# Optimization experiments

Measured on AMD Instinct MI355X. Metric: run time of the kernel, lower is better.

## Reference

```python
import jax, jax.numpy as jnp
import numpy as np

N = 100000       # nodes
E = 3200000      # edges (before self loops)
EMB = 16         # embedding dim (EMB_SIZE)
H = 32           # hidden_size
NUM_EMB = 141
EDGE_DIM = 1     # NUM_EDGE_FEATURES
NEG_SLOPE = 0.2  # PyG GATConv default negative_slope


def setup_inputs() -> dict:
    key = jax.random.key(0)
    ks = jax.random.split(key, 18)
    f32 = jnp.float32
    return {
        "x_idx": jax.random.randint(ks[0], (N, 1), 0, NUM_EMB),
        "edge_index": jax.random.randint(ks[1], (2, E), 0, N),
        "edge_attr": jax.random.normal(ks[2], (E, EDGE_DIM), f32),
        # learned params
        "emb": jax.random.normal(ks[3], (NUM_EMB, EMB), f32) * 0.1,
        # conv1 (GATConv 16->32, heads=1, edge_dim=1)
        "W1": jax.random.normal(ks[4], (EMB, H), f32) * (1.0 / np.sqrt(EMB)),
        "as1": jax.random.normal(ks[5], (H,), f32) * 0.1,
        "ad1": jax.random.normal(ks[6], (H,), f32) * 0.1,
        "We1": jax.random.normal(ks[7], (EDGE_DIM, H), f32),
        "ae1": jax.random.normal(ks[8], (H,), f32) * 0.1,
        "b1": jnp.zeros((H,), f32),
        # conv2 (GATConv 32->32)
        "W2": jax.random.normal(ks[9], (H, H), f32) * (1.0 / np.sqrt(H)),
        "as2": jax.random.normal(ks[10], (H,), f32) * 0.1,
        "ad2": jax.random.normal(ks[11], (H,), f32) * 0.1,
        "We2": jax.random.normal(ks[12], (EDGE_DIM, H), f32),
        "ae2": jax.random.normal(ks[13], (H,), f32) * 0.1,
        "b2": jnp.zeros((H,), f32),
        # linear head 32->1
        "Wl": jax.random.normal(ks[14], (H, 1), f32) * (1.0 / np.sqrt(H)),
        "bl": jnp.zeros((1,), f32),
    }


def _add_self_loops(src, dst, ea):
    # PyG add_self_loops with fill_value='mean': loop edge_attr is the
    # segment-mean of incoming edge_attr per destination node.
    sums = jax.ops.segment_sum(ea, dst, num_segments=N)            # [N, EDGE_DIM]
    cnts = jax.ops.segment_sum(jnp.ones((ea.shape[0],), ea.dtype), dst, num_segments=N)
    loop_attr = sums / jnp.maximum(cnts, 1.0)[:, None]
    loop = jnp.arange(N, dtype=src.dtype)
    return (jnp.concatenate([src, loop]),
            jnp.concatenate([dst, loop]),
            jnp.concatenate([ea, loop_attr], axis=0))


def _gat_conv(x, src, dst, ea, W, a_s, a_d, We, a_e, b):
    h = x @ W                                   # [N, H]
    e = ea @ We                                 # [E2, H]
    alpha = jax.nn.leaky_relu((h @ a_s)[src] + (h @ a_d)[dst] + e @ a_e, NEG_SLOPE)
    # segment softmax over incoming edges of each dst node
    amax = jax.ops.segment_max(alpha, dst, num_segments=N)
    ex = jnp.exp(alpha - amax[dst])
    denom = jax.ops.segment_sum(ex, dst, num_segments=N)
    coef = ex / (denom[dst] + 1e-16)            # [E2]
    out = jax.ops.segment_sum(h[src] * coef[:, None], dst, num_segments=N)
    return out + b


def reference(x_idx, edge_index, edge_attr, emb, W1, as1, ad1, We1, ae1, b1,
              W2, as2, ad2, We2, ae2, b2, Wl, bl):
    src, dst, ea = _add_self_loops(edge_index[0], edge_index[1], edge_attr)
    x = emb[x_idx[:, 0]]                        # [N, EMB]
    x = _gat_conv(x, src, dst, ea, W1, as1, ad1, We1, ae1, b1)
    x = jax.nn.relu(x)                          # dropout is identity in eval mode
    x = _gat_conv(x, src, dst, ea, W2, as2, ad2, We2, ae2, b2)
    return x @ Wl + bl                          # [N, 1]
```

## Files before the change

### kernel.cpp

```cpp
#include <hip/hip_runtime.h>

#define NN 100000
#define NE 3200000
#define H 32
#define EMBD 16
#define NEMB 141
#define NEG_SLOPE 0.2f
#define CSH 7
#define CN 128
#define NCO 782
#define CAP 4608
#define LCAP 4608
#define KCH 12800
#define GA 250

__device__ __forceinline__ float bf2f(unsigned short u) {
    return __int_as_float((int)u << 16);
}

__global__ void k_tab(const float* __restrict__ emb, const float* __restrict__ W1,
                      const float* __restrict__ as1, const float* __restrict__ ad1,
                      const float* We1, const float* ae1,
                      const float* We2, const float* ae2,
                      const float* W2, const float* as2, const float* ad2,
                      const float* Wl, const float* b2, const float* bl,
                      float* tabH, float* tabS, float* tabD, float* scal,
                      float* was2, float* wad2, float* wl2, float* c0,
                      int* bcnt) {
    int gid = blockIdx.x * 64 + threadIdx.x;
    if (gid < NCO) bcnt[gid] = 0;
    int r = blockIdx.x, j = threadIdx.x;
    if (j >= 32) {
        if (r == 0 && j == 32) {
            float c1 = 0.f, c2 = 0.f;
            for (int k = 0; k < H; k++) {
                c1 += We1[k] * ae1[k];
                c2 += We2[k] * ae2[k];
            }
            scal[0] = c1; scal[1] = c2;
        }
        if (r == 1) {
            int k = j - 32;
            float s = 0.f, d = 0.f, l = 0.f;
            for (int q = 0; q < H; q++) {
                float w = W2[k * H + q];
                s += w * as2[q];
                d += w * ad2[q];
                l += w * Wl[q];
            }
            was2[k] = s; wad2[k] = d; wl2[k] = l;
        }
        if (r == 2 && j == 32) {
            float c = bl[0];
            for (int q = 0; q < H; q++) c += b2[q] * Wl[q];
            c0[0] = c;
        }
        return;
    }
    float acc = 0.f;
    #pragma unroll
    for (int k = 0; k < EMBD; k++) acc += emb[r * EMBD + k] * W1[k * H + j];
    tabH[r * H + j] = acc;
    float s = acc * as1[j];
    float d = acc * ad1[j];
    #pragma unroll
    for (int off = 16; off > 0; off >>= 1) {
        s += __shfl_down(s, off, 32);
        d += __shfl_down(d, off, 32);
    }
    if (j == 0) { tabS[r] = s; tabD[r] = d; }
}

__global__ __launch_bounds__(1024) void k_pscat(
                        const int* __restrict__ src, const int* __restrict__ dst,
                        const float* __restrict__ ea, const int* __restrict__ x_idx,
                        int* bcnt, long long* epk) {
    __shared__ long long st[KCH];
    __shared__ unsigned short cbuk[KCH];
    __shared__ int hist[NCO];
    __shared__ int scanb[1024];
    __shared__ int bas[NCO];
    __shared__ int allow[NCO];
    int t = threadIdx.x;
    int e0 = blockIdx.x * KCH;
    const int4*   d4 = (const int4*)(dst + e0);
    const int4*   s4 = (const int4*)(src + e0);
    const float4* a4 = (const float4*)(ea + e0);
    if (t < NCO) hist[t] = 0;
    __syncthreads();

    long long pkr[4][4];
    int       pcr[4][4];
    #pragma unroll
    for (int g = 0; g < 4; g++) {
        bool v = (g < 3) || (t < 128);
        if (v) {
            int gi = g * 1024 + t;
            int4 d = d4[gi];
            int4 s = s4[gi];
            float4 a = a4[gi];
            int x0 = x_idx[s.x], x1 = x_idx[s.y], x2 = x_idx[s.z], x3 = x_idx[s.w];
            int c0 = d.x >> CSH, c1 = d.y >> CSH, c2 = d.z >> CSH, c3 = d.w >> CSH;
            pkr[g][0] = ((long long)(unsigned)__float_as_int(a.x) << 32)
                      | (unsigned)(s.x | ((d.x & (CN - 1)) << 17) | (x0 << 24));
            pkr[g][1] = ((long long)(unsigned)__float_as_int(a.y) << 32)
                      | (unsigned)(s.y | ((d.y & (CN - 1)) << 17) | (x1 << 24));
            pkr[g][2] = ((long long)(unsigned)__float_as_int(a.z) << 32)
                      | (unsigned)(s.z | ((d.z & (CN - 1)) << 17) | (x2 << 24));
            pkr[g][3] = ((long long)(unsigned)__float_as_int(a.w) << 32)
                      | (unsigned)(s.w | ((d.w & (CN - 1)) << 17) | (x3 << 24));
            pcr[g][0] = (c0 << 14) | atomicAdd(&hist[c0], 1);
            pcr[g][1] = (c1 << 14) | atomicAdd(&hist[c1], 1);
            pcr[g][2] = (c2 << 14) | atomicAdd(&hist[c2], 1);
            pcr[g][3] = (c3 << 14) | atomicAdd(&hist[c3], 1);
        }
    }
    __syncthreads();

    int hv = (t < NCO) ? hist[t] : 0;
    scanb[t] = hv;
    __syncthreads();
    for (int s = 1; s < 1024; s <<= 1) {
        int x = (t >= s) ? scanb[t - s] : 0;
        __syncthreads();
        scanb[t] += x;
        __syncthreads();
    }
    scanb[t] -= hv;
    if (t < NCO) {
        if (hv) {
            int b = atomicAdd(&bcnt[t], hv);
            bas[t]   = t * CAP + b;
            allow[t] = CAP - b;
        } else {
            bas[t] = t * CAP; allow[t] = 0;
        }
    }
    __syncthreads();

    #pragma unroll
    for (int g = 0; g < 4; g++) {
        bool v = (g < 3) || (t < 128);
        if (v) {
            #pragma unroll
            for (int e = 0; e < 4; e++) {
                int c = pcr[g][e] >> 14;
                int r = pcr[g][e] & 0x3fff;
                int pos = scanb[c] + r;
                st[pos] = pkr[g][e];
                cbuk[pos] = (unsigned short)c;
            }
        }
    }
    __syncthreads();

    for (int i = t; i < KCH; i += 1024) {
        int c = cbuk[i];
        int l = i - scanb[c];
        if (l < allow[c]) epk[bas[c] + l] = st[i];
    }
}

__global__ void k_psort(const int* __restrict__ bcnt, long long* epk, int2* nfo) {
    __shared__ long long st[LCAP];
    __shared__ unsigned short rnk[LCAP];
    __shared__ int hist[CN], lofs[CN];
    int c = blockIdx.x, t = threadIdx.x;
    int base = c * CAP;
    int cnt = bcnt[c];
    if (cnt > CAP) cnt = CAP;
    if (t < CN) hist[t] = 0;
    __syncthreads();
    for (int k = t; k < cnt; k += 512) {
        long long pk = epk[base + k];
        st[k] = pk;
        rnk[k] = (unsigned short)atomicAdd(&hist[((int)pk >> 17) & (CN - 1)], 1);
    }
    __syncthreads();
    if (t < CN) lofs[t] = hist[t];
    __syncthreads();
    for (int s = 1; s < CN; s <<= 1) {
        int x = (t >= s && t < CN) ? lofs[t - s] : 0;
        __syncthreads();
        if (t < CN) lofs[t] += x;
        __syncthreads();
    }
    if (t < CN) {
        int ex = lofs[t] - hist[t];
        lofs[t] = ex;
        int node = c * CN + t;
        if (node < NN) nfo[node] = make_int2(base + ex, hist[t]);
    }
    __syncthreads();
    for (int k = t; k < cnt; k += 512) {
        long long pk = st[k];
        int ln = ((int)pk >> 17) & (CN - 1);
        epk[base + lofs[ln] + rnk[k]] = pk;
    }
}

__global__ void k_agg1(const int2* __restrict__ nfo, const long long* __restrict__ epk,
                       const float* __restrict__ tabS, const float* __restrict__ tabD,
                       const float* __restrict__ scal,
                       const float* __restrict__ tabH,
                       const int* __restrict__ xi,
                       const float* __restrict__ bias,
                       const float* __restrict__ was2, const float* __restrict__ wad2,
                       const float* __restrict__ wl2,
                       float2* __restrict__ g2, float* __restrict__ hd2) {
    int lane = threadIdx.x & 31;
    int node = (blockIdx.x * blockDim.x + threadIdx.x) >> 5;
    if (node >= NN) return;
    int2 fo = nfo[node];
    int beg = fo.x;
    int dg  = fo.y;
    int end = beg + dg;
    float sc = scal[0];
    int xin = xi[node];
    float hdi = tabD[xin];

    float suma = 0.f, denp = 0.f, acc = 0.f;
    int base = beg;
    for (; end - base > 16; base += 32) {
        int kk = base + lane;
        int pw = 0;
        if (kk < end) {
            long long pk = epk[kk];
            int lo = (int)pk;
            float a = __int_as_float((int)(pk >> 32));
            suma += a;
            float hsv = tabS[(lo >> 24) & 0xff];
            float al = hsv + hdi + sc * a;
            al = (al > 0.f) ? al : NEG_SLOPE * al;
            int eb = __float_as_int(__expf(al));
            pw = ((eb + 0x80) & 0xffffff00) | ((lo >> 24) & 0xff);
            denp += __int_as_float(pw & 0xffffff00);
        }
        #pragma unroll
        for (int t = 0; t < 32; t++) {
            int p = __shfl(pw, t, 32);
            float ext = __int_as_float(p & 0xffffff00);
            float hv  = tabH[(p & 0xff) * H + lane];
            acc += ext * hv;
        }
    }
    if (base < end) {
        int kk = base + lane;
        int pw = 0;
        if (kk < end) {
            long long pk = epk[kk];
            int lo = (int)pk;
            float a = __int_as_float((int)(pk >> 32));
            suma += a;
            float hsv = tabS[(lo >> 24) & 0xff];
            float al = hsv + hdi + sc * a;
            al = (al > 0.f) ? al : NEG_SLOPE * al;
            int eb = __float_as_int(__expf(al));
            pw = ((eb + 0x80) & 0xffffff00) | ((lo >> 24) & 0xff);
            denp += __int_as_float(pw & 0xffffff00);
        }
        #pragma unroll
        for (int t = 0; t < 16; t++) {
            int p = __shfl(pw, t, 32);
            float ext = __int_as_float(p & 0xffffff00);
            float hv  = tabH[(p & 0xff) * H + lane];
            acc += ext * hv;
        }
    }
    #pragma unroll
    for (int o = 16; o > 0; o >>= 1) {
        suma += __shfl_xor(suma, o, 32);
        denp += __shfl_xor(denp, o, 32);
    }
    float la = suma / (float)((dg > 0) ? dg : 1);
    float alself = tabS[xin] + hdi + sc * la;
    alself = (alself > 0.f) ? alself : NEG_SLOPE * alself;
    float exs = __expf(alself);
    acc += exs * tabH[xin * H + lane];
    float den = denp + exs + 1e-16f;
    float u = acc / den;

    float x = fmaxf(u + bias[lane], 0.f);
    float sp = x * was2[lane];
    float dp = x * wad2[lane];
    float yp = x * wl2[lane];
    #pragma unroll
    for (int o = 16; o > 0; o >>= 1) {
        sp += __shfl_xor(sp, o, 32);
        dp += __shfl_xor(dp, o, 32);
        yp += __shfl_xor(yp, o, 32);
    }
    if (lane == 0) { g2[node] = make_float2(sp, yp); hd2[node] = dp; }
}

__global__ void k_agg2(const int2* __restrict__ nfo, const long long* __restrict__ epk,
                       const float2* __restrict__ g2, const float* __restrict__ hd2,
                       const float* __restrict__ scal, const float* __restrict__ c0p,
                       float* __restrict__ outF) {
    int lane = threadIdx.x & 31;
    int node = (blockIdx.x * blockDim.x + threadIdx.x) >> 5;
    if (node >= NN) return;
    int2 fo = nfo[node];
    int beg = fo.x;
    int dg  = fo.y;
    int end = beg + dg;
    float sc = scal[1];
    float hdi = hd2[node];
    float2 gn = g2[node];

    float num = 0.f, den = 0.f, suma = 0.f;
    for (int base = beg; base < end; base += 32) {
        int kk = base + lane;
        if (kk < end) {
            long long pk = epk[kk];
            float a = __int_as_float((int)(pk >> 32));
            int s = (int)pk & 0x1ffff;
            float2 g = g2[s];
            suma += a;
            float al = g.x + hdi + sc * a;
            al = (al > 0.f) ? al : NEG_SLOPE * al;
            float ex = __expf(al);
            num += ex * g.y;
            den += ex;
        }
    }
    #pragma unroll
    for (int o = 16; o > 0; o >>= 1) {
        num  += __shfl_xor(num, o, 32);
        den  += __shfl_xor(den, o, 32);
        suma += __shfl_xor(suma, o, 32);
    }
    float la = suma / (float)((dg > 0) ? dg : 1);
    float als = gn.x + hdi + sc * la;
    als = (als > 0.f) ? als : NEG_SLOPE * als;
    float exs = __expf(als);
    num += exs * gn.y;
    den += exs + 1e-16f;
    if (lane == 0) outF[node] = num / den + c0p[0];
}

extern "C" void kernel_launch(void* const* d_in, const int* in_sizes, int n_in,
                              void* d_out, int out_size, void* d_ws, size_t ws_size,
                              hipStream_t stream) {
    const int*   x_idx = (const int*)d_in[0];
    const int*   src   = (const int*)d_in[1];
    const int*   dst   = src + NE;
    const float* ea    = (const float*)d_in[2];
    const float* emb = (const float*)d_in[3];
    const float* W1  = (const float*)d_in[4];
    const float* as1 = (const float*)d_in[5];
    const float* ad1 = (const float*)d_in[6];
    const float* We1 = (const float*)d_in[7];
    const float* ae1 = (const float*)d_in[8];
    const float* b1  = (const float*)d_in[9];
    const float* W2  = (const float*)d_in[10];
    const float* as2 = (const float*)d_in[11];
    const float* ad2 = (const float*)d_in[12];
    const float* We2 = (const float*)d_in[13];
    const float* ae2 = (const float*)d_in[14];
    const float* b2  = (const float*)d_in[15];
    const float* Wl  = (const float*)d_in[16];
    const float* bl  = (const float*)d_in[17];
    float* out = (float*)d_out;

    float* ws   = (float*)d_ws;
    float* scal = ws;
    float* tabS = ws + 8;
    float* tabD = ws + 256;
    float* tabH = ws + 512;
    int*   bcnt = (int*)(ws + 5120);
    float* was2 = ws + 6144;
    float* wad2 = ws + 6208;
    float* wl2  = ws + 6272;
    float* c0   = ws + 6336;
    int2*  nfo = (int2*)(ws + 208192);
    float2* g2 = (float2*)(ws + 408192);
    long long* epk = (long long*)(ws + 2008192);
    float* hd2 = ws + 9315104;

    const int B = 256;
    int gA = (NN * H + B - 1) / B;

    k_tab<<<NEMB, 64, 0, stream>>>(emb, W1, as1, ad1, We1, ae1, We2, ae2,
                                   W2, as2, ad2, Wl, b2, bl,
                                   tabH, tabS, tabD, scal,
                                   was2, wad2, wl2, c0, bcnt);
    k_pscat<<<GA, 1024, 0, stream>>>(src, dst, ea, x_idx, bcnt, epk);
    k_psort<<<NCO, 512, 0, stream>>>(bcnt, epk, nfo);
    k_agg1<<<gA, B, 0, stream>>>(nfo, epk, tabS, tabD, scal, tabH,
                                 x_idx, b1, was2, wad2, wl2, g2, hd2);
    k_agg2<<<gA, B, 0, stream>>>(nfo, epk, g2, hd2, scal, c0, out);
}
```

Baseline: 223.6 us.

## Use 8 lanes per node with float4 feature loads in layer-1 aggregation

Layer-1 aggregation now gives each node an 8-lane group instead of 32 lanes. Each lane handles 4 edges' attention weights and owns 4 hidden features, which it loads as a float4 from the embedding table. The edge broadcast is done with ds_swizzle inside the 8-lane group instead of a full 32-lane shuffle, and the grid shrinks by 4x. This cuts the shuffle and reduction overhead and the idle lanes on low-degree nodes, at the cost of more registers per thread and more serial work per lane.

```diff
diff --git a/kernel.cpp b/kernel.cpp
--- a/kernel.cpp
+++ b/kernel.cpp
@@ -1,4 +1,5 @@
 #include <hip/hip_runtime.h>
+#include <utility>
 
 #define NN 100000
 #define NE 3200000
@@ -16,6 +17,15 @@
 
 __device__ __forceinline__ float bf2f(unsigned short u) {
     return __int_as_float((int)u << 16);
+}
+
+template<class F, int... Is>
+__device__ __forceinline__ void static_for_impl(F f, std::integer_sequence<int, Is...>) {
+    (f(std::integral_constant<int, Is>{}), ...);
+}
+template<int N, class F>
+__device__ __forceinline__ void static_for(F f) {
+    static_for_impl(f, std::make_integer_sequence<int, N>{});
 }
 
 __global__ void k_tab(const float* __restrict__ emb, const float* __restrict__ W1,
@@ -208,8 +218,8 @@
                        const float* __restrict__ was2, const float* __restrict__ wad2,
                        const float* __restrict__ wl2,
                        float2* __restrict__ g2, float* __restrict__ hd2) {
-    int lane = threadIdx.x & 31;
-    int node = (blockIdx.x * blockDim.x + threadIdx.x) >> 5;
+    int ln   = threadIdx.x & 7;
+    int node = (blockIdx.x * blockDim.x + threadIdx.x) >> 3;
     if (node >= NN) return;
     int2 fo = nfo[node];
     int beg = fo.x;
@@ -219,78 +229,102 @@
     int xin = xi[node];
     float hdi = tabD[xin];
 
-    float suma = 0.f, denp = 0.f, acc = 0.f;
+    float suma = 0.f, denp = 0.f;
+    float4 acc = make_float4(0.f, 0.f, 0.f, 0.f);
     int base = beg;
     for (; end - base > 16; base += 32) {
-        int kk = base + lane;
-        int pw = 0;
-        if (kk < end) {
-            long long pk = epk[kk];
-            int lo = (int)pk;
-            float a = __int_as_float((int)(pk >> 32));
-            suma += a;
-            float hsv = tabS[(lo >> 24) & 0xff];
-            float al = hsv + hdi + sc * a;
-            al = (al > 0.f) ? al : NEG_SLOPE * al;
-            int eb = __float_as_int(__expf(al));
-            pw = ((eb + 0x80) & 0xffffff00) | ((lo >> 24) & 0xff);
-            denp += __int_as_float(pw & 0xffffff00);
-        }
+        int pw[4] = {0, 0, 0, 0};
         #pragma unroll
-        for (int t = 0; t < 32; t++) {
-            int p = __shfl(pw, t, 32);
+        for (int e = 0; e < 4; e++) {
+            int kk = base + 4 * ln + e;
+            if (kk < end) {
+                long long pk = epk[kk];
+                int lo = (int)pk;
+                float a = __int_as_float((int)(pk >> 32));
+                suma += a;
+                float hsv = tabS[(lo >> 24) & 0xff];
+                float al = hsv + hdi + sc * a;
+                al = (al > 0.f) ? al : NEG_SLOPE * al;
+                int eb = __float_as_int(__expf(al));
+                pw[e] = ((eb + 0x80) & 0xffffff00) | ((lo >> 24) & 0xff);
+                denp += __int_as_float(pw[e] & 0xffffff00);
+            }
+        }
+        static_for<32>([&](auto tc) {
+            constexpr int t = decltype(tc)::value;
+            int p = __builtin_amdgcn_ds_swizzle(pw[t & 3], ((t >> 2) << 5) | 0x18);
             float ext = __int_as_float(p & 0xffffff00);
-            float hv  = tabH[(p & 0xff) * H + lane];
-            acc += ext * hv;
-        }
+            const float4 hv = *(const float4*)(tabH + ((p & 0xff) << 5) + (ln << 2));
+            acc.x += ext * hv.x;
+            acc.y += ext * hv.y;
+            acc.z += ext * hv.z;
+            acc.w += ext * hv.w;
+        });
     }
     if (base < end) {
-        int kk = base + lane;
-        int pw = 0;
-        if (kk < end) {
-            long long pk = epk[kk];
-            int lo = (int)pk;
-            float a = __int_as_float((int)(pk >> 32));
-            suma += a;
-            float hsv = tabS[(lo >> 24) & 0xff];
-            float al = hsv + hdi + sc * a;
-            al = (al > 0.f) ? al : NEG_SLOPE * al;
-            int eb = __float_as_int(__expf(al));
-            pw = ((eb + 0x80) & 0xffffff00) | ((lo >> 24) & 0xff);
-            denp += __int_as_float(pw & 0xffffff00);
-        }
+        int pw[2] = {0, 0};
         #pragma unroll
-        for (int t = 0; t < 16; t++) {
-            int p = __shfl(pw, t, 32);
+        for (int e = 0; e < 2; e++) {
+            int kk = base + 2 * ln + e;
+            if (kk < end) {
+                long long pk = epk[kk];
+                int lo = (int)pk;
+                float a = __int_as_float((int)(pk >> 32));
+                suma += a;
+                float hsv = tabS[(lo >> 24) & 0xff];
+                float al = hsv + hdi + sc * a;
+                al = (al > 0.f) ? al : NEG_SLOPE * al;
+                int eb = __float_as_int(__expf(al));
+                pw[e] = ((eb + 0x80) & 0xffffff00) | ((lo >> 24) & 0xff);
+                denp += __int_as_float(pw[e] & 0xffffff00);
+            }
+        }
+        static_for<16>([&](auto tc) {
+            constexpr int t = decltype(tc)::value;
+            int p = __builtin_amdgcn_ds_swizzle(pw[t & 1], ((t >> 1) << 5) | 0x18);
             float ext = __int_as_float(p & 0xffffff00);
-            float hv  = tabH[(p & 0xff) * H + lane];
-            acc += ext * hv;
-        }
-    }
-    #pragma unroll
-    for (int o = 16; o > 0; o >>= 1) {
-        suma += __shfl_xor(suma, o, 32);
-        denp += __shfl_xor(denp, o, 32);
+            const float4 hv = *(const float4*)(tabH + ((p & 0xff) << 5) + (ln << 2));
+            acc.x += ext * hv.x;
+            acc.y += ext * hv.y;
+            acc.z += ext * hv.z;
+            acc.w += ext * hv.w;
+        });
+    }
+    #pragma unroll
+    for (int o = 4; o > 0; o >>= 1) {
+        suma += __shfl_xor(suma, o, 8);
+        denp += __shfl_xor(denp, o, 8);
     }
     float la = suma / (float)((dg > 0) ? dg : 1);
     float alself = tabS[xin] + hdi + sc * la;
     alself = (alself > 0.f) ? alself : NEG_SLOPE * alself;
     float exs = __expf(alself);
-    acc += exs * tabH[xin * H + lane];
+    const float4 hvs = *(const float4*)(tabH + (xin << 5) + (ln << 2));
+    acc.x += exs * hvs.x;
+    acc.y += exs * hvs.y;
+    acc.z += exs * hvs.z;
+    acc.w += exs * hvs.w;
     float den = denp + exs + 1e-16f;
-    float u = acc / den;
-
-    float x = fmaxf(u + bias[lane], 0.f);
-    float sp = x * was2[lane];
-    float dp = x * wad2[lane];
-    float yp = x * wl2[lane];
-    #pragma unroll
-    for (int o = 16; o > 0; o >>= 1) {
-        sp += __shfl_xor(sp, o, 32);
-        dp += __shfl_xor(dp, o, 32);
-        yp += __shfl_xor(yp, o, 32);
-    }
-    if (lane == 0) { g2[node] = make_float2(sp, yp); hd2[node] = dp; }
+
+    const float4 b4 = *(const float4*)(bias + (ln << 2));
+    float4 x;
+    x.x = fmaxf(acc.x / den + b4.x, 0.f);
+    x.y = fmaxf(acc.y / den + b4.y, 0.f);
+    x.z = fmaxf(acc.z / den + b4.z, 0.f);
+    x.w = fmaxf(acc.w / den + b4.w, 0.f);
+    const float4 wa = *(const float4*)(was2 + (ln << 2));
+    const float4 wd = *(const float4*)(wad2 + (ln << 2));
+    const float4 wy = *(const float4*)(wl2  + (ln << 2));
+    float sp = x.x * wa.x + x.y * wa.y + x.z * wa.z + x.w * wa.w;
+    float dp = x.x * wd.x + x.y * wd.y + x.z * wd.z + x.w * wd.w;
+    float yp = x.x * wy.x + x.y * wy.y + x.z * wy.z + x.w * wy.w;
+    #pragma unroll
+    for (int o = 4; o > 0; o >>= 1) {
+        sp += __shfl_xor(sp, o, 8);
+        dp += __shfl_xor(dp, o, 8);
+        yp += __shfl_xor(yp, o, 8);
+    }
+    if (ln == 0) { g2[node] = make_float2(sp, yp); hd2[node] = dp; }
 }
 
 __global__ void k_agg2(const int2* __restrict__ nfo, const long long* __restrict__ epk,
@@ -379,7 +413,8 @@
     float* hd2 = ws + 9315104;
 
     const int B = 256;
-    int gA = (NN * H + B - 1) / B;
+    int g1 = (NN * 8 + B - 1) / B;
+    int g2g = (NN * H + B - 1) / B;
 
     k_tab<<<NEMB, 64, 0, stream>>>(emb, W1, as1, ad1, We1, ae1, We2, ae2,
                                    W2, as2, ad2, Wl, b2, bl,
@@ -387,7 +422,7 @@
                                    was2, wad2, wl2, c0, bcnt);
     k_pscat<<<GA, 1024, 0, stream>>>(src, dst, ea, x_idx, bcnt, epk);
     k_psort<<<NCO, 512, 0, stream>>>(bcnt, epk, nfo);
-    k_agg1<<<gA, B, 0, stream>>>(nfo, epk, tabS, tabD, scal, tabH,
+    k_agg1<<<g1, B, 0, stream>>>(nfo, epk, tabS, tabD, scal, tabH,
                                  x_idx, b1, was2, wad2, wl2, g2, hd2);
-    k_agg2<<<gA, B, 0, stream>>>(nfo, epk, g2, hd2, scal, c0, out);
-}
+    k_agg2<<<g2g, B, 0, stream>>>(nfo, epk, g2, hd2, scal, c0, out);
+}
```

New measurement: 214.8 us. 3.9% less time.
